# Performance work log

Measured on AMD Instinct MI355X. Metric: run time of the kernel, lower is better.

## Reference

```python
import jax, jax.numpy as jnp
import numpy as np

NUM_HEADS = 16
EPS = 1e-6


def setup_inputs() -> dict:
    key = jax.random.key(0)
    k1, k2, k3 = jax.random.split(key, 3)
    B, S, D = 4, 4096, 1024
    x = jax.random.normal(k1, (B, S, D), dtype=jnp.float32)
    # weights scaled like nn.Linear init (~1/sqrt(fan_in))
    Wqkv = jax.random.normal(k2, (D, 3 * D), dtype=jnp.float32) / np.sqrt(D)
    Wo = jax.random.normal(k3, (D, D), dtype=jnp.float32) / np.sqrt(D)
    return {"x": x, "Wqkv": Wqkv, "Wo": Wo}


def reference(x, Wqkv, Wo):
    B, S, D = x.shape
    H = NUM_HEADS
    hd = D // H
    qkv = x @ Wqkv                                   # [B,S,3D]
    qkv = qkv.reshape(B, S, 3, H, hd).transpose(2, 0, 3, 1, 4)
    Q, K, V = qkv[0], qkv[1], qkv[2]                 # [B,H,S,hd]
    # feature map: elu(x) + 1 (positive)
    Q = jax.nn.elu(Q) + 1.0
    K = jax.nn.elu(K) + 1.0
    # O(N d^2): KV state then Q contraction
    KV = jnp.einsum('bhnd,bhnv->bhdv', K, V)         # [B,H,hd,hd]
    out = jnp.einsum('bhnd,bhdv->bhnv', Q, KV)       # [B,H,S,hd]
    K_sum = K.sum(axis=2)                            # [B,H,hd]
    normalizer = jnp.einsum('bhnd,bhd->bhn', Q, K_sum)[..., None]  # [B,H,S,1]
    out = out / (normalizer + EPS)
    out = out.transpose(0, 2, 1, 3).reshape(B, S, D)
    return out @ Wo
```

## Files before the change

kernel.cpp:

```cpp
#include <hip/hip_runtime.h>

using u16 = unsigned short;
typedef __attribute__((ext_vector_type(8))) short short8;
typedef __attribute__((ext_vector_type(4))) float f32x4;

__device__ __forceinline__ u16 f2bf(float f) {
  unsigned int u = __float_as_uint(f);
  u = (u + 0x7FFFu + ((u >> 16) & 1u)) >> 16;
  return (u16)u;
}
__device__ __forceinline__ float bf2f(u16 v) {
  return __uint_as_float(((unsigned int)v) << 16);
}

__device__ __forceinline__ void gload16(const void* g, void* l) {
  __builtin_amdgcn_global_load_lds((const __attribute__((address_space(1))) void*)g,
                                   (__attribute__((address_space(3))) void*)l, 16, 0, 0);
}

#define B_ 4
#define S_ 4096
#define D_ 1024
#define H_ 16
#define HD_ 64
#define M_ (B_*S_)
#define N1_ (3*D_)

#define OFF_XB    0ull
#define OFF_WQKVT (OFF_XB    + (size_t)M_*D_*2)
#define OFF_WOT   (OFF_WQKVT + (size_t)N1_*D_*2)
#define OFF_QBUF  (OFF_WOT   + (size_t)D_*D_*2)
#define OFF_KT    (OFF_QBUF  + (size_t)M_*D_*2)
#define OFF_VT    (OFF_KT    + (size_t)M_*D_*2)
#define OFF_KV    (OFF_VT    + (size_t)M_*D_*2)
#define OFF_KSUM  (OFF_KV    + (size_t)4*64*4096*4)
#define WS_NEEDED (OFF_KSUM  + (size_t)4*64*64*4)
#define OFF_WT    OFF_KT
#define OFF_KVS   (OFF_KT + ((size_t)8<<20))
#define OFF_KSG   (OFF_KT + ((size_t)9<<20))
#define OFF_KVPP  OFF_VT
#define OFF_KSPP  (OFF_VT + ((size_t)16<<20))

__global__ __launch_bounds__(256) void prep_kernel(const float* __restrict__ x, u16* __restrict__ xb,
                                                   const float* __restrict__ Wqkv, u16* __restrict__ wqkvt,
                                                   const float* __restrict__ Wo, u16* __restrict__ wot)
{
  __shared__ float tile[32][33];
  int bid = blockIdx.x, tid = threadIdx.x;
  if (bid < 16384) {
    int i = bid * 256 + tid;
    float4 v = ((const float4*)x)[i];
    uint2 o;
    o.x = (unsigned)f2bf(v.x) | ((unsigned)f2bf(v.y) << 16);
    o.y = (unsigned)f2bf(v.z) | ((unsigned)f2bf(v.w) << 16);
    ((uint2*)xb)[i] = o;
    return;
  }
  const float* in; u16* out; int R, C, cb, rb;
  if (bid < 19456) {
    int t = bid - 16384;  in = Wqkv; out = wqkvt; R = D_; C = N1_;
    cb = t % 96; rb = t / 96;
  } else {
    int t = bid - 19456;  in = Wo; out = wot; R = D_; C = D_;
    cb = t % 32; rb = t / 32;
  }
  int tx = tid & 31, ty = tid >> 5;
  int c0 = cb * 32, r0 = rb * 32;
#pragma unroll
  for (int i = 0; i < 4; i++)
    tile[ty + i*8][tx] = in[(size_t)(r0 + ty + i*8) * C + c0 + tx];
  __syncthreads();
#pragma unroll
  for (int i = 0; i < 4; i++)
    out[(size_t)(c0 + ty + i*8) * R + r0 + tx] = f2bf(tile[tx][ty + i*8]);
}

template<int MODE>
__global__ __launch_bounds__(512, 2) void gemm256(
    const u16* __restrict__ A, const u16* __restrict__ Bt,
    float* __restrict__ Cf, u16* __restrict__ qout,
    float* __restrict__ P1, float* __restrict__ P2,
    int M, int N, int K)
{
  __shared__ __align__(16) char smem[131072];
  int tid = threadIdx.x;
  int w = tid >> 6, lane = tid & 63;
  int quad = lane >> 4, l16 = lane & 15;
  int wm = w >> 2, wn = w & 3;

  int nwg = gridDim.x * gridDim.y;
  int flat = blockIdx.y * gridDim.x + blockIdx.x;
  int wg = (flat & 7) * (nwg >> 3) + (flat >> 3);
  int bx = wg % gridDim.x, by = wg / gridDim.x;
  int bm = by * 256, bn = bx * 256;

  int prl = lane >> 3;
  int c4  = (lane & 7) ^ prl;
  int r0  = ((w << 3) + prl) * 2 + (c4 >> 2);
  int koff = (c4 & 3) * 8;
  const u16* gA0 = A + (size_t)(bm + r0) * K + koff;
  const u16* gB0;
  size_t rowskipA = (size_t)128 * K;
  size_t rowskipB;
  if constexpr (MODE == 3) {
    gB0 = Bt + (size_t)(1024 + bx * 128 + r0) * K + koff;
    rowskipB = (size_t)1024 * K;
  } else if constexpr (MODE == 2) {
    gB0 = Bt + ((size_t)(bm >> 12) << 20) + (size_t)(bn + r0) * K + koff;
    rowskipB = (size_t)128 * K;
  } else {
    gB0 = Bt + (size_t)(bn + r0) * K + koff;
    rowskipB = (size_t)128 * K;
  }
  char* smemc = smem;
  int ldsAw = w * 1024;
  int ldsBw = 65536 + w * 1024;

  int ph = (((l16 & 1) << 2) | quad) ^ ((l16 >> 1) & 7);
  int baseA = wm * 8192 + (l16 >> 1) * 128 + ph * 16;
  int baseB = 65536 + wn * 4096 + (l16 >> 1) * 128 + ph * 16;

  f32x4 acc[8][4];
#pragma unroll
  for (int i = 0; i < 8; i++)
#pragma unroll
    for (int j = 0; j < 4; j++) acc[i][j] = (f32x4)0.0f;

  int nt = K >> 5;

#define STG(tt, slot) {                                                   \
    const u16* a0_ = gA0 + (tt) * 32;                                     \
    const u16* b0_ = gB0 + (tt) * 32;                                     \
    gload16(a0_,            smemc + (slot)*16384 + ldsAw);                \
    gload16(a0_ + rowskipA, smemc + (slot)*16384 + 8192 + ldsAw);         \
    gload16(b0_,            smemc + (slot)*16384 + ldsBw);                \
    gload16(b0_ + rowskipB, smemc + (slot)*16384 + 8192 + ldsBw);         \
  }

#define COMPUTE(slot) {                                                              \
    const char* sb = smemc + (slot) * 16384;                                         \
    short8 bfr[4], af[8];                                                            \
    _Pragma("unroll")                                                                \
    for (int nj = 0; nj < 4; nj++) bfr[nj] = *(const short8*)(sb + baseB + nj*1024); \
    _Pragma("unroll")                                                                \
    for (int mi = 0; mi < 8; mi++) af[mi] = *(const short8*)(sb + baseA + mi*1024);  \
    __builtin_amdgcn_s_setprio(1);                                                   \
    _Pragma("unroll")                                                                \
    for (int mi = 0; mi < 8; mi++)                                                   \
      _Pragma("unroll")                                                              \
      for (int nj = 0; nj < 4; nj++)                                                 \
        acc[mi][nj] = __builtin_amdgcn_mfma_f32_16x16x32_bf16(af[mi], bfr[nj],       \
                                                              acc[mi][nj], 0, 0, 0); \
    __builtin_amdgcn_s_setprio(0);                                                   \
  }

#define WAITBAR(n) {                                                      \
    asm volatile("s_waitcnt vmcnt(" #n ")" ::: "memory");                 \
    __builtin_amdgcn_s_barrier();                                         \
    asm volatile("" ::: "memory");                                        \
  }

  STG(0, 0); STG(1, 1); STG(2, 2);
  WAITBAR(8)

  for (int tb = 0; tb < nt - 4; tb += 4) {
#pragma unroll
    for (int i = 0; i < 4; ++i) {
      int t = tb + i;
      STG(t + 3, ((i + 3) & 3));
      COMPUTE(i)
      WAITBAR(8)
    }
  }

  STG(nt - 1, 3);
  COMPUTE(0)
  WAITBAR(8)
  COMPUTE(1)
  WAITBAR(4)
  COMPUTE(2)
  WAITBAR(0)
  COMPUTE(3)

#undef STG
#undef COMPUTE
#undef WAITBAR

  if constexpr (MODE == 2) {
    int colbase = bn + wn * 64;
#pragma unroll
    for (int mi = 0; mi < 8; mi++) {
      int row0 = bm + wm * 128 + mi * 16 + quad * 4;
#pragma unroll
      for (int nj = 0; nj < 4; nj++) {
        int col = colbase + nj * 16 + l16;
#pragma unroll
        for (int r = 0; r < 4; r++)
          Cf[(size_t)(row0 + r) * N + col] = acc[mi][nj][r];
      }
    }
  } else if constexpr (MODE == 1) {
#pragma unroll
    for (int mi = 0; mi < 8; mi++) {
      int row0 = bm + wm * 128 + mi * 16 + quad * 4;
#pragma unroll
      for (int nj = 0; nj < 4; nj++) {
        int col = bn + wn * 64 + nj * 16 + l16;
#pragma unroll
        for (int r = 0; r < 4; r++) {
          float v = acc[mi][nj][r];
          v = (v > 0.0f) ? (v + 1.0f) : __expf(v);
          qout[(size_t)(row0 + r) * D_ + col] = f2bf(v);
        }
      }
    }
  } else {
    __syncthreads();
    {
      char* basekv = smemc + ((wn < 2) ? 0 : 65536);
      bool doElu = (wn < 2);
#pragma unroll
      for (int mi = 0; mi < 8; mi++) {
        int sb = wm * 128 + mi * 16 + quad * 4;
        int slot = sb >> 5;
        int kc = (sb >> 3) & 3;
        int so = (sb & 7) * 2;
#pragma unroll
        for (int nj = 0; nj < 4; nj++) {
          int dv = (wn & 1) * 64 + nj * 16 + l16;
          int pc = (((dv & 1) << 2) | kc) ^ ((dv >> 1) & 7);
          float v0 = acc[mi][nj][0], v1 = acc[mi][nj][1], v2 = acc[mi][nj][2], v3 = acc[mi][nj][3];
          if (doElu) {
            v0 = (v0 > 0.0f) ? (v0 + 1.0f) : __expf(v0);
            v1 = (v1 > 0.0f) ? (v1 + 1.0f) : __expf(v1);
            v2 = (v2 > 0.0f) ? (v2 + 1.0f) : __expf(v2);
            v3 = (v3 > 0.0f) ? (v3 + 1.0f) : __expf(v3);
          }
          uint2 o;
          o.x = (unsigned)f2bf(v0) | ((unsigned)f2bf(v1) << 16);
          o.y = (unsigned)f2bf(v2) | ((unsigned)f2bf(v3) << 16);
          *(uint2*)(basekv + slot*8192 + (dv >> 1)*128 + pc*16 + so) = o;
        }
      }
    }
    __syncthreads();
    int hh = w >> 2, dh = w & 1, vh = (w >> 1) & 1;
    short8 ones;
#pragma unroll
    for (int e = 0; e < 8; ++e) ones[e] = (short)0x3F80;
    f32x4 a2[2][2], s2[2];
#pragma unroll
    for (int i = 0; i < 2; i++) {
      s2[i] = (f32x4)0.0f;
#pragma unroll
      for (int j = 0; j < 2; j++) a2[i][j] = (f32x4)0.0f;
    }
#pragma unroll
    for (int t = 0; t < 8; t++) {
      short8 ak[2], bv[2];
#pragma unroll
      for (int i = 0; i < 2; i++) {
        int d = hh * 64 + dh * 32 + i * 16 + l16;
        ak[i] = *(const short8*)(smemc + t*8192 + (d >> 1)*128 +
                                 (((((d & 1) << 2) | quad)) ^ ((d >> 1) & 7))*16);
        int v = hh * 64 + vh * 32 + i * 16 + l16;
        bv[i] = *(const short8*)(smemc + 65536 + t*8192 + (v >> 1)*128 +
                                 (((((v & 1) << 2) | quad)) ^ ((v >> 1) & 7))*16);
      }
#pragma unroll
      for (int i = 0; i < 2; i++) {
#pragma unroll
        for (int j = 0; j < 2; j++)
          a2[i][j] = __builtin_amdgcn_mfma_f32_16x16x32_bf16(ak[i], bv[j], a2[i][j], 0, 0, 0);
        if (vh == 0)
          s2[i] = __builtin_amdgcn_mfma_f32_16x16x32_bf16(ak[i], ones, s2[i], 0, 0, 0);
      }
    }
    int p = bx;
    int mb = bm >> 8;
    float* kdst = P1 + (size_t)(mb * 16 + p * 2 + hh) * 4096;
#pragma unroll
    for (int i = 0; i < 2; i++)
#pragma unroll
      for (int j = 0; j < 2; j++)
#pragma unroll
        for (int r = 0; r < 4; r++)
          kdst[(dh*32 + i*16 + quad*4 + r) * 64 + vh*32 + j*16 + l16] = a2[i][j][r];
    if (vh == 0 && l16 == 0) {
      float* sdst = P2 + (size_t)(mb * 16 + p * 2 + hh) * 64;
#pragma unroll
      for (int i = 0; i < 2; i++)
#pragma unroll
        for (int r = 0; r < 4; r++)
          sdst[dh*32 + i*16 + quad*4 + r] = s2[i][r];
    }
  }
}

__global__ __launch_bounds__(256) void kvsum_kernel(const float* __restrict__ kvpp,
                                                    const float* __restrict__ kspp,
                                                    float* __restrict__ kvp,
                                                    float* __restrict__ ksg)
{
  int tid = threadIdx.x, bh = blockIdx.x;
  int b = bh >> 4, phh = bh & 15;
  int base = b * 256 + phh;
  for (int i = tid; i < 4096; i += 256) {
    float s = 0.0f;
#pragma unroll
    for (int m = 0; m < 16; ++m)
      s += kvpp[(size_t)(base + m * 16) * 4096 + i];
    kvp[(size_t)bh * 4096 + i] = s;
  }
  if (tid < 64) {
    float s = 0.0f;
#pragma unroll
    for (int m = 0; m < 16; ++m)
      s += kspp[(size_t)(base + m * 16) * 64 + tid];
    ksg[bh * 64 + tid] = s;
  }
}

__global__ __launch_bounds__(256) void kvw_kernel(const float* __restrict__ kvp,
                                                  const u16* __restrict__ wot,
                                                  u16* __restrict__ wt)
{
  __shared__ u16 kvlds[4096];
  int tid = threadIdx.x;
  int ct = blockIdx.x;
  int bh = blockIdx.y;
  int b = bh >> 4, h = bh & 15;
  const float* kvsrc = kvp + (size_t)bh * 4096;
  for (int i = tid; i < 4096; i += 256) kvlds[i] = f2bf(kvsrc[i]);
  __syncthreads();
  int w = tid >> 6, lane = tid & 63, quad = lane >> 4, l16 = lane & 15;

  short8 bfr[2][4];
#pragma unroll
  for (int ks = 0; ks < 2; ++ks)
#pragma unroll
    for (int nj = 0; nj < 4; ++nj)
      bfr[ks][nj] = *(const short8*)(&kvlds[(nj*16 + l16) * 64 + ks*32 + quad*8]);

  f32x4 acc[2][4];
#pragma unroll
  for (int i = 0; i < 2; i++)
#pragma unroll
    for (int j = 0; j < 4; j++) acc[i][j] = (f32x4)0.0f;

  int c0 = ct * 128 + w * 32;
#pragma unroll
  for (int ks = 0; ks < 2; ++ks) {
#pragma unroll
    for (int mi = 0; mi < 2; ++mi) {
      short8 af = *(const short8*)(wot + (size_t)(c0 + mi*16 + l16) * 1024 + h*64 + ks*32 + quad*8);
#pragma unroll
      for (int nj = 0; nj < 4; ++nj)
        acc[mi][nj] = __builtin_amdgcn_mfma_f32_16x16x32_bf16(af, bfr[ks][nj], acc[mi][nj], 0, 0, 0);
    }
  }
  u16* dst = wt + ((size_t)b << 20);
#pragma unroll
  for (int mi = 0; mi < 2; ++mi) {
    int c = c0 + mi*16 + quad*4;
#pragma unroll
    for (int nj = 0; nj < 4; ++nj) {
      int hd = h*64 + nj*16 + l16;
#pragma unroll
      for (int r = 0; r < 4; ++r)
        dst[(size_t)(c + r) * 1024 + hd] = f2bf(acc[mi][nj][r]);
    }
  }
}

__global__ __launch_bounds__(256) void qscale_kernel(u16* __restrict__ qbuf,
                                                     const float* __restrict__ ksum)
{
  __shared__ float ks[1024];
  int tid = threadIdx.x;
  int blk = blockIdx.x;
  int b = blk >> 10;
  for (int i = tid; i < 1024; i += 256) ks[i] = ksum[b * 1024 + i];
  __syncthreads();
  int wv = tid >> 6, ln = tid & 63;
  int s = blk * 4 + wv;
  u16* row = qbuf + (size_t)s * 1024 + ln * 16;
  short8 qa = *(const short8*)row;
  short8 qb = *(const short8*)(row + 8);
  int h4 = (ln >> 2) * 64 + (ln & 3) * 16;
  float p = 0.0f;
#pragma unroll
  for (int j = 0; j < 8; ++j) p += bf2f((u16)qa[j]) * ks[h4 + j];
#pragma unroll
  for (int j = 0; j < 8; ++j) p += bf2f((u16)qb[j]) * ks[h4 + 8 + j];
  p += __shfl_xor(p, 1);
  p += __shfl_xor(p, 2);
  float inv = 1.0f / (p + 1e-6f);
  short8 oa, ob;
#pragma unroll
  for (int j = 0; j < 8; ++j) {
    oa[j] = (short)f2bf(bf2f((u16)qa[j]) * inv);
    ob[j] = (short)f2bf(bf2f((u16)qb[j]) * inv);
  }
  *(short8*)row = oa;
  *(short8*)(row + 8) = ob;
}

extern "C" void kernel_launch(void* const* d_in, const int* in_sizes, int n_in,
                              void* d_out, int out_size, void* d_ws, size_t ws_size,
                              hipStream_t stream) {
  const float* x    = (const float*)d_in[0];
  const float* Wqkv = (const float*)d_in[1];
  const float* Wo   = (const float*)d_in[2];
  float* out = (float*)d_out;
  char* ws = (char*)d_ws;
  if (ws_size < WS_NEEDED) return;

  u16*   xb    = (u16*)  (ws + OFF_XB);
  u16*   wqkvt = (u16*)  (ws + OFF_WQKVT);
  u16*   wot   = (u16*)  (ws + OFF_WOT);
  u16*   qbuf  = (u16*)  (ws + OFF_QBUF);
  u16*   wt    = (u16*)  (ws + OFF_WT);
  float* kvs   = (float*)(ws + OFF_KVS);
  float* ksg   = (float*)(ws + OFF_KSG);
  float* kvpp  = (float*)(ws + OFF_KVPP);
  float* kspp  = (float*)(ws + OFF_KSPP);

  prep_kernel<<<20480, 256, 0, stream>>>(x, xb, Wqkv, wqkvt, Wo, wot);
  gemm256<3><<<dim3(8, M_/256), 512, 0, stream>>>(xb, wqkvt, nullptr, nullptr, kvpp, kspp,
                                                  M_, N1_, D_);
  gemm256<1><<<dim3(4, M_/256), 512, 0, stream>>>(xb, wqkvt, nullptr, qbuf, nullptr, nullptr,
                                                  M_, N1_, D_);
  kvsum_kernel<<<64, 256, 0, stream>>>(kvpp, kspp, kvs, ksg);
  kvw_kernel<<<dim3(8, 64), 256, 0, stream>>>(kvs, wot, wt);
  qscale_kernel<<<4096, 256, 0, stream>>>(qbuf, ksg);
  gemm256<2><<<dim3(4, M_/256), 512, 0, stream>>>(qbuf, wt, out, nullptr, nullptr, nullptr,
                                                  M_, D_, D_);
}
```

Measured before the change: 293.2 us.

## Fuse Q normalizer into Q GEMM epilogue and merge KV reduction with KV·Wo

The K/V GEMM now runs first, so the summed K vector is available when the Q projection GEMM runs. The Q GEMM epilogue computes the per-row, per-head normalizer with cross-lane shuffles and writes pre-scaled Q, which removes the separate qscale pass over the Q buffer. The partial-sum reduction kernel is merged into the KV·Wo kernel, which keeps the reduced KV in LDS instead of writing it to global memory. The cost is a much smaller grid for the merged kernel (64 blocks instead of 512), which may leave it with too little parallelism.

New measurement: 288.7 us. No clear change (-1.5%).

```diff
diff --git a/kernel.cpp b/kernel.cpp
--- a/kernel.cpp
+++ b/kernel.cpp
@@ -36,7 +36,6 @@
 #define OFF_KSUM  (OFF_KV    + (size_t)4*64*4096*4)
 #define WS_NEEDED (OFF_KSUM  + (size_t)4*64*64*4)
 #define OFF_WT    OFF_KT
-#define OFF_KVS   (OFF_KT + ((size_t)8<<20))
 #define OFF_KSG   (OFF_KT + ((size_t)9<<20))
 #define OFF_KVPP  OFF_VT
 #define OFF_KSPP  (OFF_VT + ((size_t)16<<20))
@@ -80,6 +79,7 @@
     const u16* __restrict__ A, const u16* __restrict__ Bt,
     float* __restrict__ Cf, u16* __restrict__ qout,
     float* __restrict__ P1, float* __restrict__ P2,
+    const float* __restrict__ Ks,
     int M, int N, int K)
 {
   __shared__ __align__(16) char smem[131072];
@@ -199,19 +199,43 @@
           Cf[(size_t)(row0 + r) * N + col] = acc[mi][nj][r];
       }
     }
-  } else if constexpr (MODE == 1) {
+  } else if constexpr (MODE == 4) {
+    int colbase = bn + wn * 64;
+    int b = bm >> 12;
+    int h = colbase >> 6;
+    float ksv[4];
+#pragma unroll
+    for (int nj = 0; nj < 4; nj++)
+      ksv[nj] = Ks[(b * 16 + h) * 64 + nj * 16 + l16];
 #pragma unroll
     for (int mi = 0; mi < 8; mi++) {
-      int row0 = bm + wm * 128 + mi * 16 + quad * 4;
-#pragma unroll
-      for (int nj = 0; nj < 4; nj++) {
-        int col = bn + wn * 64 + nj * 16 + l16;
+      float vv[4][4], nrm[4];
+#pragma unroll
+      for (int r = 0; r < 4; r++) nrm[r] = 0.0f;
+#pragma unroll
+      for (int nj = 0; nj < 4; nj++)
 #pragma unroll
         for (int r = 0; r < 4; r++) {
           float v = acc[mi][nj][r];
           v = (v > 0.0f) ? (v + 1.0f) : __expf(v);
-          qout[(size_t)(row0 + r) * D_ + col] = f2bf(v);
+          vv[nj][r] = v;
+          nrm[r] += v * ksv[nj];
         }
+#pragma unroll
+      for (int r = 0; r < 4; r++) {
+        nrm[r] += __shfl_xor(nrm[r], 1);
+        nrm[r] += __shfl_xor(nrm[r], 2);
+        nrm[r] += __shfl_xor(nrm[r], 4);
+        nrm[r] += __shfl_xor(nrm[r], 8);
+        nrm[r] = 1.0f / (nrm[r] + 1e-6f);
+      }
+      int row0 = bm + wm * 128 + mi * 16 + quad * 4;
+#pragma unroll
+      for (int nj = 0; nj < 4; nj++) {
+        int col = colbase + nj * 16 + l16;
+#pragma unroll
+        for (int r = 0; r < 4; r++)
+          qout[(size_t)(row0 + r) * D_ + col] = f2bf(vv[nj][r] * nrm[r]);
       }
     }
   } else {
@@ -297,41 +321,29 @@
   }
 }
 
-__global__ __launch_bounds__(256) void kvsum_kernel(const float* __restrict__ kvpp,
-                                                    const float* __restrict__ kspp,
-                                                    float* __restrict__ kvp,
-                                                    float* __restrict__ ksg)
+__global__ __launch_bounds__(512) void kvw_kernel(const float* __restrict__ kvpp,
+                                                  const float* __restrict__ kspp,
+                                                  const u16* __restrict__ wot,
+                                                  u16* __restrict__ wt,
+                                                  float* __restrict__ ksg)
 {
+  __shared__ u16 kvlds[4096];
   int tid = threadIdx.x, bh = blockIdx.x;
-  int b = bh >> 4, phh = bh & 15;
-  int base = b * 256 + phh;
-  for (int i = tid; i < 4096; i += 256) {
+  int b = bh >> 4, h = bh & 15;
+  for (int i = tid; i < 4096; i += 512) {
     float s = 0.0f;
 #pragma unroll
     for (int m = 0; m < 16; ++m)
-      s += kvpp[(size_t)(base + m * 16) * 4096 + i];
-    kvp[(size_t)bh * 4096 + i] = s;
+      s += kvpp[(size_t)(((b * 16 + m) * 16) + h) * 4096 + i];
+    kvlds[i] = f2bf(s);
   }
   if (tid < 64) {
     float s = 0.0f;
 #pragma unroll
     for (int m = 0; m < 16; ++m)
-      s += kspp[(size_t)(base + m * 16) * 64 + tid];
+      s += kspp[(size_t)(((b * 16 + m) * 16) + h) * 64 + tid];
     ksg[bh * 64 + tid] = s;
   }
-}
-
-__global__ __launch_bounds__(256) void kvw_kernel(const float* __restrict__ kvp,
-                                                  const u16* __restrict__ wot,
-                                                  u16* __restrict__ wt)
-{
-  __shared__ u16 kvlds[4096];
-  int tid = threadIdx.x;
-  int ct = blockIdx.x;
-  int bh = blockIdx.y;
-  int b = bh >> 4, h = bh & 15;
-  const float* kvsrc = kvp + (size_t)bh * 4096;
-  for (int i = tid; i < 4096; i += 256) kvlds[i] = f2bf(kvsrc[i]);
   __syncthreads();
   int w = tid >> 6, lane = tid & 63, quad = lane >> 4, l16 = lane & 15;
 
@@ -342,68 +354,37 @@
     for (int nj = 0; nj < 4; ++nj)
       bfr[ks][nj] = *(const short8*)(&kvlds[(nj*16 + l16) * 64 + ks*32 + quad*8]);
 
-  f32x4 acc[2][4];
-#pragma unroll
-  for (int i = 0; i < 2; i++)
-#pragma unroll
-    for (int j = 0; j < 4; j++) acc[i][j] = (f32x4)0.0f;
-
-  int c0 = ct * 128 + w * 32;
-#pragma unroll
-  for (int ks = 0; ks < 2; ++ks) {
+  u16* dst = wt + ((size_t)b << 20);
+#pragma unroll
+  for (int cc = 0; cc < 4; ++cc) {
+    int c0 = w * 128 + cc * 32;
+    f32x4 acc[2][4];
+#pragma unroll
+    for (int i = 0; i < 2; i++)
+#pragma unroll
+      for (int j = 0; j < 4; j++) acc[i][j] = (f32x4)0.0f;
+#pragma unroll
+    for (int ks = 0; ks < 2; ++ks) {
+#pragma unroll
+      for (int mi = 0; mi < 2; ++mi) {
+        short8 af = *(const short8*)(wot + (size_t)(c0 + mi*16 + l16) * 1024 + h*64 + ks*32 + quad*8);
+#pragma unroll
+        for (int nj = 0; nj < 4; ++nj)
+          acc[mi][nj] = __builtin_amdgcn_mfma_f32_16x16x32_bf16(af, bfr[ks][nj], acc[mi][nj], 0, 0, 0);
+      }
+    }
 #pragma unroll
     for (int mi = 0; mi < 2; ++mi) {
-      short8 af = *(const short8*)(wot + (size_t)(c0 + mi*16 + l16) * 1024 + h*64 + ks*32 + quad*8);
-#pragma unroll
-      for (int nj = 0; nj < 4; ++nj)
-        acc[mi][nj] = __builtin_amdgcn_mfma_f32_16x16x32_bf16(af, bfr[ks][nj], acc[mi][nj], 0, 0, 0);
-    }
-  }
-  u16* dst = wt + ((size_t)b << 20);
-#pragma unroll
-  for (int mi = 0; mi < 2; ++mi) {
-    int c = c0 + mi*16 + quad*4;
-#pragma unroll
-    for (int nj = 0; nj < 4; ++nj) {
-      int hd = h*64 + nj*16 + l16;
-#pragma unroll
-      for (int r = 0; r < 4; ++r)
-        dst[(size_t)(c + r) * 1024 + hd] = f2bf(acc[mi][nj][r]);
-    }
-  }
-}
-
-__global__ __launch_bounds__(256) void qscale_kernel(u16* __restrict__ qbuf,
-                                                     const float* __restrict__ ksum)
-{
-  __shared__ float ks[1024];
-  int tid = threadIdx.x;
-  int blk = blockIdx.x;
-  int b = blk >> 10;
-  for (int i = tid; i < 1024; i += 256) ks[i] = ksum[b * 1024 + i];
-  __syncthreads();
-  int wv = tid >> 6, ln = tid & 63;
-  int s = blk * 4 + wv;
-  u16* row = qbuf + (size_t)s * 1024 + ln * 16;
-  short8 qa = *(const short8*)row;
-  short8 qb = *(const short8*)(row + 8);
-  int h4 = (ln >> 2) * 64 + (ln & 3) * 16;
-  float p = 0.0f;
-#pragma unroll
-  for (int j = 0; j < 8; ++j) p += bf2f((u16)qa[j]) * ks[h4 + j];
-#pragma unroll
-  for (int j = 0; j < 8; ++j) p += bf2f((u16)qb[j]) * ks[h4 + 8 + j];
-  p += __shfl_xor(p, 1);
-  p += __shfl_xor(p, 2);
-  float inv = 1.0f / (p + 1e-6f);
-  short8 oa, ob;
-#pragma unroll
-  for (int j = 0; j < 8; ++j) {
-    oa[j] = (short)f2bf(bf2f((u16)qa[j]) * inv);
-    ob[j] = (short)f2bf(bf2f((u16)qb[j]) * inv);
-  }
-  *(short8*)row = oa;
-  *(short8*)(row + 8) = ob;
+      int c = c0 + mi*16 + quad*4;
+#pragma unroll
+      for (int nj = 0; nj < 4; ++nj) {
+        int hd = h*64 + nj*16 + l16;
+#pragma unroll
+        for (int r = 0; r < 4; ++r)
+          dst[(size_t)(c + r) * 1024 + hd] = f2bf(acc[mi][nj][r]);
+      }
+    }
+  }
 }
 
 extern "C" void kernel_launch(void* const* d_in, const int* in_sizes, int n_in,
@@ -421,19 +402,16 @@
   u16*   wot   = (u16*)  (ws + OFF_WOT);
   u16*   qbuf  = (u16*)  (ws + OFF_QBUF);
   u16*   wt    = (u16*)  (ws + OFF_WT);
-  float* kvs   = (float*)(ws + OFF_KVS);
   float* ksg   = (float*)(ws + OFF_KSG);
   float* kvpp  = (float*)(ws + OFF_KVPP);
   float* kspp  = (float*)(ws + OFF_KSPP);
 
   prep_kernel<<<20480, 256, 0, stream>>>(x, xb, Wqkv, wqkvt, Wo, wot);
   gemm256<3><<<dim3(8, M_/256), 512, 0, stream>>>(xb, wqkvt, nullptr, nullptr, kvpp, kspp,
-                                                  M_, N1_, D_);
-  gemm256<1><<<dim3(4, M_/256), 512, 0, stream>>>(xb, wqkvt, nullptr, qbuf, nullptr, nullptr,
-                                                  M_, N1_, D_);
-  kvsum_kernel<<<64, 256, 0, stream>>>(kvpp, kspp, kvs, ksg);
-  kvw_kernel<<<dim3(8, 64), 256, 0, stream>>>(kvs, wot, wt);
-  qscale_kernel<<<4096, 256, 0, stream>>>(qbuf, ksg);
+                                                  nullptr, M_, N1_, D_);
+  kvw_kernel<<<64, 512, 0, stream>>>(kvpp, kspp, wot, wt, ksg);
+  gemm256<4><<<dim3(4, M_/256), 512, 0, stream>>>(xb, wqkvt, nullptr, qbuf, nullptr, nullptr,
+                                                  ksg, M_, N1_, D_);
   gemm256<2><<<dim3(4, M_/256), 512, 0, stream>>>(qbuf, wt, out, nullptr, nullptr, nullptr,
-                                                  M_, D_, D_);
-}
+                                                  nullptr, M_, D_, D_);
+}
```
